# Kernel optimization log

Hardware: AMD Instinct MI355X
Metric: run time of the kernel (lower is better)

## Reference

```python
import jax, jax.numpy as jnp
import numpy as np
import math

B, T, C = 2, 2048, 1024
H = 16
HD = C // H  # 64
LAMBDA_INIT = 0.7 - 0.6 * math.exp(-0.3 * (2 - 1))
EPS = 1e-5


def setup_inputs() -> dict:
    key = jax.random.key(0)
    ks = jax.random.split(key, 12)
    s = 1.0 / math.sqrt(C)
    return {
        'x':   jax.random.normal(ks[0], (B, T, C), jnp.float32),
        'Wq1': jax.random.normal(ks[1], (C, C), jnp.float32) * s,
        'Wq2': jax.random.normal(ks[2], (C, C), jnp.float32) * s,
        'Wk1': jax.random.normal(ks[3], (C, C), jnp.float32) * s,
        'Wk2': jax.random.normal(ks[4], (C, C), jnp.float32) * s,
        'Wv':  jax.random.normal(ks[5], (2 * C, C), jnp.float32) * s,
        'Wc':  jax.random.normal(ks[6], (C, 2 * C), jnp.float32) * (1.0 / math.sqrt(2 * C)),
        'lq1': jax.random.normal(ks[7], (H, HD), jnp.float32) * 0.1,
        'lk1': jax.random.normal(ks[8], (H, HD), jnp.float32) * 0.1,
        'lq2': jax.random.normal(ks[9], (H, HD), jnp.float32) * 0.1,
        'lk2': jax.random.normal(ks[10], (H, HD), jnp.float32) * 0.1,
    }


def _heads(x, W, d):
    # x:[B,T,C] @ W.T:[C,out] -> [B,H,T,d]
    b, t, _ = x.shape
    return jnp.einsum('btc,dc->btd', x, W).reshape(b, t, H, d).transpose(0, 2, 1, 3)


def reference(x, Wq1, Wq2, Wk1, Wk2, Wv, Wc, lq1, lk1, lq2, lk2):
    b, t, c = x.shape
    q1 = _heads(x, Wq1, HD)
    q2 = _heads(x, Wq2, HD)
    k1 = _heads(x, Wk1, HD)
    k2 = _heads(x, Wk2, HD)
    v = _heads(x, Wv, 2 * HD)  # [B,H,T,2hd]
    scale = 1.0 / math.sqrt(HD)
    causal = jnp.tril(jnp.ones((t, t), bool))  # [T,T]
    neg = jnp.float32(-jnp.inf)
    att1 = jnp.einsum('bhqd,bhkd->bhqk', q1, k1) * scale
    att2 = jnp.einsum('bhqd,bhkd->bhqk', q2, k2) * scale
    att1 = jax.nn.softmax(jnp.where(causal, att1, neg), axis=-1)
    att2 = jax.nn.softmax(jnp.where(causal, att2, neg), axis=-1)
    lam1 = jnp.exp(jnp.sum(lq1 * lk1, -1))  # [H]
    lam2 = jnp.exp(jnp.sum(lq2 * lk2, -1))
    lam_full = (lam1 - lam2 + LAMBDA_INIT)[None, :, None, None]
    att = att1 - lam_full * att2
    y = jnp.einsum('bhqk,bhkd->bhqd', att, v)  # [B,H,T,2hd]
    # sub-layernorm over last dim, no affine
    mu = jnp.mean(y, -1, keepdims=True)
    var = jnp.mean(jnp.square(y - mu), -1, keepdims=True)
    y = (y - mu) * jax.lax.rsqrt(var + EPS)
    y = y * (1.0 - LAMBDA_INIT)
    y = y.transpose(0, 2, 1, 3).reshape(b, t, 2 * c)
    return jnp.einsum('btd,cd->btc', y, Wc)
```

## Files before the change

kernel.cpp:

```cpp
#include <hip/hip_runtime.h>
#include <stdint.h>

typedef unsigned short u16;
typedef unsigned int   u32;
typedef short  short8  __attribute__((ext_vector_type(8)));
typedef float  f32x4   __attribute__((ext_vector_type(4)));
typedef u16    u16x4   __attribute__((ext_vector_type(4)));
typedef u32    u32x4   __attribute__((ext_vector_type(4)));

#define LAMBDA_INIT   0.25550906759096927f
#define ONE_MINUS_LI  0.7444909324090307f
#define QSCALE        0.18033688011112043f

__device__ __forceinline__ u16 f2bf(float f) {
  union { float f; u32 u; } v; v.f = f;
  u32 r = v.u + 0x7fffu + ((v.u >> 16) & 1u);
  return (u16)(r >> 16);
}

__device__ __forceinline__ u32 packtr(float a, float b) {
  return (__builtin_bit_cast(u32, a) >> 16) | (__builtin_bit_cast(u32, b) & 0xffff0000u);
}

__device__ __forceinline__ float expv(float x) {
  float r; asm("v_exp_f32 %0, %1" : "=v"(r) : "v"(x)); return r;
}

__device__ __forceinline__ void gload16(const void* g, void* l) {
  __builtin_amdgcn_global_load_lds(
      (const __attribute__((address_space(1))) void*)g,
      (__attribute__((address_space(3))) void*)l, 16, 0, 0);
}

__global__ __launch_bounds__(256) void k_cvt(const float* __restrict__ s,
                                             u16* __restrict__ d, int n) {
  int i = (blockIdx.x * 256 + threadIdx.x) * 4;
  if (i >= n) return;
  float4 v = *(const float4*)(s + i);
  u16x4 o = { f2bf(v.x), f2bf(v.y), f2bf(v.z), f2bf(v.w) };
  *(u16x4*)(d + i) = o;
}

__global__ __launch_bounds__(256) void k_cvt4(
    const float* __restrict__ s0, const float* __restrict__ s1,
    const float* __restrict__ s2, const float* __restrict__ s3,
    u16* __restrict__ d) {
  const float* s = (blockIdx.y == 0) ? s0 : (blockIdx.y == 1) ? s1
                 : (blockIdx.y == 2) ? s2 : s3;
  int i = (blockIdx.x * 256 + threadIdx.x) * 4;
  float4 v = *(const float4*)(s + i);
  u16x4 o = { f2bf(v.x), f2bf(v.y), f2bf(v.z), f2bf(v.w) };
  *(u16x4*)(d + blockIdx.y * 1048576 + i) = o;
}

__device__ __forceinline__ void gemm_tile_128(
    const u16* __restrict__ A, const u16* __restrict__ Bm, int K,
    int m0, int n0, char* smem, f32x4 acc[4][4]) {
  const int tid = threadIdx.x;
  const int l = tid & 63, w = tid >> 6, g = l >> 4, q = l & 15;
  const int wm = w >> 1, wn = w & 1;
  char* As = smem;
  char* Bs = smem + 16384;
#pragma unroll
  for (int mi = 0; mi < 4; mi++)
#pragma unroll
    for (int ni = 0; ni < 4; ni++) acc[mi][ni] = (f32x4){0.f, 0.f, 0.f, 0.f};

  const int nkt = K >> 6;
  for (int kt = 0; kt < nkt; ++kt) {
    __syncthreads();
#pragma unroll
    for (int i = 0; i < 4; i++) {
      int cc = i * 256 + tid;
      int row = cc >> 3, off = cc & 7;
      int sw = (off * 16) ^ ((row & 7) << 4);
      gload16((const char*)A + ((size_t)(m0 + row) * K + kt * 64) * 2 + sw, As + cc * 16);
      gload16((const char*)Bm + ((size_t)(n0 + row) * K + kt * 64) * 2 + sw, Bs + cc * 16);
    }
    __syncthreads();
#pragma unroll
    for (int ks = 0; ks < 2; ++ks) {
      short8 af[4], bf[4];
#pragma unroll
      for (int mi = 0; mi < 4; mi++) {
        int row = wm * 64 + mi * 16 + q;
        af[mi] = *(const short8*)(As + ((row * 128 + ks * 64 + g * 16) ^ ((row & 7) << 4)));
      }
#pragma unroll
      for (int ni = 0; ni < 4; ni++) {
        int row = wn * 64 + ni * 16 + q;
        bf[ni] = *(const short8*)(Bs + ((row * 128 + ks * 64 + g * 16) ^ ((row & 7) << 4)));
      }
#pragma unroll
      for (int mi = 0; mi < 4; mi++)
#pragma unroll
        for (int ni = 0; ni < 4; ni++)
          acc[mi][ni] = __builtin_amdgcn_mfma_f32_16x16x32_bf16(af[mi], bf[ni], acc[mi][ni], 0, 0, 0);
    }
  }
}

__global__ __launch_bounds__(256) void k_gemm_qkv(
    const u16* __restrict__ xb, const u16* __restrict__ wall,
    u16* __restrict__ q1, u16* __restrict__ q2,
    u16* __restrict__ k1, u16* __restrict__ k2,
    u16* __restrict__ vt) {
  __shared__ __align__(16) char smem[32768];
  f32x4 acc[4][4];
  const int n0 = blockIdx.x * 128, m0 = blockIdx.y * 128;
  gemm_tile_128(xb, wall, 1024, m0, n0, smem, acc);

  const int l = threadIdx.x & 63, w = threadIdx.x >> 6, g = l >> 4, q = l & 15;
  const int wm = w >> 1, wn = w & 1;
  const int seg = n0 >> 10;
  const float sc = (seg < 2) ? QSCALE : 1.0f;
  u16* qk = (seg == 0) ? q1 : (seg == 1) ? q2 : (seg == 2) ? k1 : k2;
#pragma unroll
  for (int mi = 0; mi < 4; mi++)
#pragma unroll
    for (int ni = 0; ni < 4; ni++) {
      int row0 = m0 + wm * 64 + mi * 16 + 4 * g;
      int col = n0 + wn * 64 + ni * 16 + q;
      int bb = row0 >> 11;
      if (seg < 4) {
        int h = (col >> 6) & 15, hd = col & 63;
#pragma unroll
        for (int r = 0; r < 4; r++) {
          int t = (row0 + r) & 2047;
          qk[(((size_t)bb * 16 + h) * 2048 + t) * 64 + hd] = f2bf(acc[mi][ni][r] * sc);
        }
      } else {
        int nv = col - 4096, hh = nv >> 7, d = nv & 127;
        int t = row0 & 2047;
        u16x4 pv;
#pragma unroll
        for (int r = 0; r < 4; r++) pv[r] = f2bf(acc[mi][ni][r]);
        size_t addr = (size_t)(bb * 16 + hh) * 262144 + (size_t)(t >> 6) * 8192
                    + (size_t)(((((t >> 5) & 1) * 8 + (d >> 4)) * 512)
                               + ((t >> 3) & 3) * 128 + (d & 15) * 8 + (t & 7));
        *(u16x4*)(vt + addr) = pv;
      }
    }
}

__global__ __launch_bounds__(256) void k_attn(
    const u16* __restrict__ q1p, const u16* __restrict__ q2p,
    const u16* __restrict__ k1p, const u16* __restrict__ k2p,
    const u16* __restrict__ vfp,
    const float* __restrict__ lq1, const float* __restrict__ lk1,
    const float* __restrict__ lq2, const float* __restrict__ lk2,
    u16* __restrict__ ybp) {
  __shared__ __align__(16) char smem[65536];
  const int bh = blockIdx.y, b = bh >> 4, h = bh & 15;
  const int tid = threadIdx.x, w = tid >> 6, l = tid & 63, g = l >> 4, q = l & 15;
  const int xA = blockIdx.x;
  const int nA = xA + 1;

  float a1 = lq1[h * 64 + l] * lk1[h * 64 + l];
  float a2 = lq2[h * 64 + l] * lk2[h * 64 + l];
#pragma unroll
  for (int off = 32; off; off >>= 1) {
    a1 += __shfl_xor(a1, off);
    a2 += __shfl_xor(a2, off);
  }
  const float lam = expf(a1) - expf(a2) + LAMBDA_INIT;

  short8 qf[2][2];
  f32x4 o[2][8];
  float lsum[2];
  int qrow = 0;

  auto init_tile = [&](int q0) {
    qrow = q0 + w * 16 + q;
    size_t qoff = ((size_t)bh * 2048 + qrow) * 64;
#pragma unroll
    for (int ks = 0; ks < 2; ++ks) {
      qf[0][ks] = *(const short8*)(q1p + qoff + ks * 32 + g * 8);
      qf[1][ks] = *(const short8*)(q2p + qoff + ks * 32 + g * 8);
    }
#pragma unroll
    for (int s = 0; s < 2; s++) {
      lsum[s] = 0.f;
#pragma unroll
      for (int mt = 0; mt < 8; mt++) o[s][mt] = (f32x4){0.f, 0.f, 0.f, 0.f};
    }
  };

  auto stage_kv = [&](char* sb, int kv0) {
#pragma unroll
    for (int i = 0; i < 2; i++) {
      int cc = i * 256 + tid, kv = cc >> 3, off = cc & 7;
      int sw = (off * 16) ^ ((kv & 7) << 4);
      size_t rb = ((size_t)bh * 2048 + kv0 + kv) * 128;
      gload16((const char*)k1p + rb + sw, sb + cc * 16);
      gload16((const char*)k2p + rb + sw, sb + 8192 + cc * 16);
    }
    const char* vsrc = (const char*)vfp + (size_t)bh * 524288 + (size_t)(kv0 >> 6) * 16384;
#pragma unroll
    for (int i = 0; i < 4; i++) {
      int cc = i * 256 + tid;
      gload16(vsrc + cc * 16, sb + 16384 + cc * 16);
    }
  };

  auto epilogue = [&]() {
    float l0 = lsum[0]; l0 += __shfl_xor(l0, 16); l0 += __shfl_xor(l0, 32);
    float l1 = lsum[1]; l1 += __shfl_xor(l1, 16); l1 += __shfl_xor(l1, 32);
    const float inv0 = 1.f / l0, inv1 = 1.f / l1;
    float sum = 0.f, ssq = 0.f;
#pragma unroll
    for (int mt = 0; mt < 8; ++mt)
#pragma unroll
      for (int r = 0; r < 4; r++) {
        float y = o[0][mt][r] * inv0 - lam * (o[1][mt][r] * inv1);
        o[0][mt][r] = y;
        sum += y;
        ssq += y * y;
      }
    sum += __shfl_xor(sum, 16); sum += __shfl_xor(sum, 32);
    ssq += __shfl_xor(ssq, 16); ssq += __shfl_xor(ssq, 32);
    const float mean = sum * (1.f / 128.f);
    const float var = ssq * (1.f / 128.f) - mean * mean;
    const float rstd = rsqrtf(var + 1e-5f) * ONE_MINUS_LI;
    u16* dst = ybp + ((size_t)(b * 2048 + qrow)) * 2048 + h * 128;
#pragma unroll
    for (int mt = 0; mt < 8; ++mt) {
      u16x4 pv;
#pragma unroll
      for (int r = 0; r < 4; r++) pv[r] = f2bf((o[0][mt][r] - mean) * rstd);
      *(u16x4*)(dst + mt * 16 + 4 * g) = pv;
    }
  };

  init_tile(xA * 64);
  stage_kv(smem, 0);

  for (int i = 0; i < 33; ++i) {
    char* sb = smem + (i & 1) * 32768;
    asm volatile("s_waitcnt vmcnt(0)" ::: "memory");
    __builtin_amdgcn_s_barrier();
    if (i + 1 < 33) {
      int kvn = (i + 1 < nA) ? (i + 1) * 64 : (i + 1 - nA) * 64;
      stage_kv(smem + ((i + 1) & 1) * 32768, kvn);
    }

    const int kv0 = (i < nA) ? i * 64 : (i - nA) * 64;
    const bool diag = (i == nA - 1) || (i == 32);

#pragma unroll
    for (int kk = 0; kk < 2; ++kk) {
      u32 pk[2][4];
#pragma unroll
      for (int s = 0; s < 2; ++s) {
        const char* Ks = sb + s * 8192;
        f32x4 s0 = {0.f, 0.f, 0.f, 0.f}, s1 = {0.f, 0.f, 0.f, 0.f};
#pragma unroll
        for (int ks = 0; ks < 2; ++ks) {
          short8 af0 = *(const short8*)(Ks + (((kk * 32 + q) * 128 + ks * 64 + g * 16) ^ ((q & 7) << 4)));
          short8 af1 = *(const short8*)(Ks + (((kk * 32 + 16 + q) * 128 + ks * 64 + g * 16) ^ ((q & 7) << 4)));
          s0 = __builtin_amdgcn_mfma_f32_16x16x32_bf16(af0, qf[s][ks], s0, 0, 0, 0);
          s1 = __builtin_amdgcn_mfma_f32_16x16x32_bf16(af1, qf[s][ks], s1, 0, 0, 0);
        }
        const int kb0 = kv0 + kk * 32 + 4 * g, kb1 = kb0 + 16;
        if (diag) {
#pragma unroll
          for (int r = 0; r < 4; r++) {
            s0[r] = (kb0 + r > qrow) ? -1e30f : s0[r];
            s1[r] = (kb1 + r > qrow) ? -1e30f : s1[r];
          }
        }
        float p0[4], p1[4], rs = 0.f;
#pragma unroll
        for (int r = 0; r < 4; r++) {
          p0[r] = expv(s0[r]);
          p1[r] = expv(s1[r]);
          rs += p0[r] + p1[r];
        }
        lsum[s] += rs;

        u32 pk0[2] = { packtr(p0[0], p0[1]), packtr(p0[2], p0[3]) };
        u32 pk1[2] = { packtr(p1[0], p1[1]), packtr(p1[2], p1[3]) };
        int srcA = q + (g & 1) * 32;
        int srcB = srcA + 16;
        u32 xa0 = (u32)__shfl((int)pk0[0], srcA), xa1 = (u32)__shfl((int)pk0[1], srcA);
        u32 xa2 = (u32)__shfl((int)pk0[0], srcB), xa3 = (u32)__shfl((int)pk0[1], srcB);
        u32 xb0 = (u32)__shfl((int)pk1[0], srcA), xb1 = (u32)__shfl((int)pk1[1], srcA);
        u32 xb2 = (u32)__shfl((int)pk1[0], srcB), xb3 = (u32)__shfl((int)pk1[1], srcB);
        bool lo = (g < 2);
        pk[s][0] = lo ? xa0 : xb0;
        pk[s][1] = lo ? xa1 : xb1;
        pk[s][2] = lo ? xa2 : xb2;
        pk[s][3] = lo ? xa3 : xb3;
      }
      u32x4 t0 = {pk[0][0], pk[0][1], pk[0][2], pk[0][3]};
      u32x4 t1 = {pk[1][0], pk[1][1], pk[1][2], pk[1][3]};
      short8 pf0 = __builtin_bit_cast(short8, t0);
      short8 pf1 = __builtin_bit_cast(short8, t1);
      const char* Vb = sb + 16384 + kk * 8192 + l * 16;
#pragma unroll
      for (int mt = 0; mt < 8; ++mt) {
        short8 vf = *(const short8*)(Vb + mt * 1024);
        o[0][mt] = __builtin_amdgcn_mfma_f32_16x16x32_bf16(vf, pf0, o[0][mt], 0, 0, 0);
        o[1][mt] = __builtin_amdgcn_mfma_f32_16x16x32_bf16(vf, pf1, o[1][mt], 0, 0, 0);
      }
    }

    if (i == nA - 1) {
      epilogue();
      init_tile((31 - xA) * 64);
    }
  }
  epilogue();
}

__global__ __launch_bounds__(256) void k_gemm_out(
    const u16* __restrict__ yb, const u16* __restrict__ wcb,
    float* __restrict__ out) {
  __shared__ __align__(16) char smem[32768];
  f32x4 acc[4][4];
  const int n0 = blockIdx.x * 128, m0 = blockIdx.y * 128;
  gemm_tile_128(yb, wcb, 2048, m0, n0, smem, acc);
  const int l = threadIdx.x & 63, w = threadIdx.x >> 6, g = l >> 4, q = l & 15;
  const int wm = w >> 1, wn = w & 1;
#pragma unroll
  for (int mi = 0; mi < 4; mi++)
#pragma unroll
    for (int ni = 0; ni < 4; ni++)
#pragma unroll
      for (int r = 0; r < 4; r++) {
        int row = m0 + wm * 64 + mi * 16 + 4 * g + r;
        int col = n0 + wn * 64 + ni * 16 + q;
        out[(size_t)row * 1024 + col] = acc[mi][ni][r];
      }
}

extern "C" void kernel_launch(void* const* d_in, const int* in_sizes, int n_in,
                              void* d_out, int out_size, void* d_ws, size_t ws_size,
                              hipStream_t stream) {
  const float* x   = (const float*)d_in[0];
  const float* Wq1 = (const float*)d_in[1];
  const float* Wq2 = (const float*)d_in[2];
  const float* Wk1 = (const float*)d_in[3];
  const float* Wk2 = (const float*)d_in[4];
  const float* Wv  = (const float*)d_in[5];
  const float* Wc  = (const float*)d_in[6];
  const float* lq1 = (const float*)d_in[7];
  const float* lk1 = (const float*)d_in[8];
  const float* lq2 = (const float*)d_in[9];
  const float* lk2 = (const float*)d_in[10];

  char* ws = (char*)d_ws;
  u16* xb   = (u16*)(ws);
  u16* wall = (u16*)(ws + 8388608);
  u16* wcb  = (u16*)(ws + 20971520);
  u16* q1   = (u16*)(ws + 25165824);
  u16* q2   = (u16*)(ws + 33554432);
  u16* k1   = (u16*)(ws + 41943040);
  u16* k2   = (u16*)(ws + 50331648);
  u16* vt   = (u16*)(ws + 58720256);
  u16* yb   = (u16*)(ws + 75497472);

  k_cvt<<<4096, 256, 0, stream>>>(x, xb, 4194304);
  k_cvt4<<<dim3(1024, 4), 256, 0, stream>>>(Wq1, Wq2, Wk1, Wk2, wall);
  k_cvt<<<2048, 256, 0, stream>>>(Wv,  wall + 4194304,  2097152);
  k_cvt<<<2048, 256, 0, stream>>>(Wc,  wcb, 2097152);

  k_gemm_qkv<<<dim3(48, 32), 256, 0, stream>>>(xb, wall, q1, q2, k1, k2, vt);
  k_attn<<<dim3(16, 32), 256, 0, stream>>>(q1, q2, k1, k2, vt,
                                           lq1, lk1, lq2, lk2, yb);
  k_gemm_out<<<dim3(8, 32), 256, 0, stream>>>(yb, wcb, (float*)d_out);
}
```

Before: 225.0 us.

## Use 512-thread attention blocks over 128-row query tiles, heavy tiles first

Before, each 256-thread block handled a pair of 64-row query tiles (x and 31-x) to balance causal work. Now each block has 8 waves covering one 128-row query tile. Tiles are scheduled in reverse order so the longest causal tiles start first, and each K/V chunk staged in shared memory is shared by twice as many query rows. Waves whose rows lie entirely before a chunk skip its compute but still join the barriers. Per-block work is now unbalanced, and the launch bounds of 512 threads with 4 blocks per CU limit registers.

Measured after the change: 473.7 us. 111% more time.

```diff
diff --git a/kernel.cpp b/kernel.cpp
--- a/kernel.cpp
+++ b/kernel.cpp
@@ -143,7 +143,7 @@
     }
 }
 
-__global__ __launch_bounds__(256) void k_attn(
+__global__ __launch_bounds__(512, 4) void k_attn(
     const u16* __restrict__ q1p, const u16* __restrict__ q2p,
     const u16* __restrict__ k1p, const u16* __restrict__ k2p,
     const u16* __restrict__ vfp,
@@ -153,8 +153,11 @@
   __shared__ __align__(16) char smem[65536];
   const int bh = blockIdx.y, b = bh >> 4, h = bh & 15;
   const int tid = threadIdx.x, w = tid >> 6, l = tid & 63, g = l >> 4, q = l & 15;
-  const int xA = blockIdx.x;
-  const int nA = xA + 1;
+  const int tile = 15 - blockIdx.x;
+  const int base = tile * 128;
+  const int nchunk = 2 * tile + 2;
+  const int qrow = base + w * 16 + q;
+  const int wqmin = base + w * 16;
 
   float a1 = lq1[h * 64 + l] * lk1[h * 64 + l];
   float a2 = lq2[h * 64 + l] * lk2[h * 64 + l];
@@ -166,86 +169,43 @@
   const float lam = expf(a1) - expf(a2) + LAMBDA_INIT;
 
   short8 qf[2][2];
-  f32x4 o[2][8];
-  float lsum[2];
-  int qrow = 0;
-
-  auto init_tile = [&](int q0) {
-    qrow = q0 + w * 16 + q;
+  {
     size_t qoff = ((size_t)bh * 2048 + qrow) * 64;
 #pragma unroll
     for (int ks = 0; ks < 2; ++ks) {
       qf[0][ks] = *(const short8*)(q1p + qoff + ks * 32 + g * 8);
       qf[1][ks] = *(const short8*)(q2p + qoff + ks * 32 + g * 8);
     }
-#pragma unroll
-    for (int s = 0; s < 2; s++) {
-      lsum[s] = 0.f;
-#pragma unroll
-      for (int mt = 0; mt < 8; mt++) o[s][mt] = (f32x4){0.f, 0.f, 0.f, 0.f};
-    }
+  }
+  f32x4 o[2][8];
+  float lsum[2] = {0.f, 0.f};
+#pragma unroll
+  for (int s = 0; s < 2; s++)
+#pragma unroll
+    for (int mt = 0; mt < 8; mt++) o[s][mt] = (f32x4){0.f, 0.f, 0.f, 0.f};
+
+  auto stage_kv = [&](char* sb, int kv0) {
+    int kv = tid >> 3, off = tid & 7;
+    int sw = (off * 16) ^ ((kv & 7) << 4);
+    size_t rb = ((size_t)bh * 2048 + kv0 + kv) * 128;
+    gload16((const char*)k1p + rb + sw, sb + tid * 16);
+    gload16((const char*)k2p + rb + sw, sb + 8192 + tid * 16);
+    const char* vsrc = (const char*)vfp + (size_t)bh * 524288 + (size_t)(kv0 >> 6) * 16384;
+    gload16(vsrc + tid * 16, sb + 16384 + tid * 16);
+    gload16(vsrc + 8192 + tid * 16, sb + 24576 + tid * 16);
   };
 
-  auto stage_kv = [&](char* sb, int kv0) {
-#pragma unroll
-    for (int i = 0; i < 2; i++) {
-      int cc = i * 256 + tid, kv = cc >> 3, off = cc & 7;
-      int sw = (off * 16) ^ ((kv & 7) << 4);
-      size_t rb = ((size_t)bh * 2048 + kv0 + kv) * 128;
-      gload16((const char*)k1p + rb + sw, sb + cc * 16);
-      gload16((const char*)k2p + rb + sw, sb + 8192 + cc * 16);
-    }
-    const char* vsrc = (const char*)vfp + (size_t)bh * 524288 + (size_t)(kv0 >> 6) * 16384;
-#pragma unroll
-    for (int i = 0; i < 4; i++) {
-      int cc = i * 256 + tid;
-      gload16(vsrc + cc * 16, sb + 16384 + cc * 16);
-    }
-  };
-
-  auto epilogue = [&]() {
-    float l0 = lsum[0]; l0 += __shfl_xor(l0, 16); l0 += __shfl_xor(l0, 32);
-    float l1 = lsum[1]; l1 += __shfl_xor(l1, 16); l1 += __shfl_xor(l1, 32);
-    const float inv0 = 1.f / l0, inv1 = 1.f / l1;
-    float sum = 0.f, ssq = 0.f;
-#pragma unroll
-    for (int mt = 0; mt < 8; ++mt)
-#pragma unroll
-      for (int r = 0; r < 4; r++) {
-        float y = o[0][mt][r] * inv0 - lam * (o[1][mt][r] * inv1);
-        o[0][mt][r] = y;
-        sum += y;
-        ssq += y * y;
-      }
-    sum += __shfl_xor(sum, 16); sum += __shfl_xor(sum, 32);
-    ssq += __shfl_xor(ssq, 16); ssq += __shfl_xor(ssq, 32);
-    const float mean = sum * (1.f / 128.f);
-    const float var = ssq * (1.f / 128.f) - mean * mean;
-    const float rstd = rsqrtf(var + 1e-5f) * ONE_MINUS_LI;
-    u16* dst = ybp + ((size_t)(b * 2048 + qrow)) * 2048 + h * 128;
-#pragma unroll
-    for (int mt = 0; mt < 8; ++mt) {
-      u16x4 pv;
-#pragma unroll
-      for (int r = 0; r < 4; r++) pv[r] = f2bf((o[0][mt][r] - mean) * rstd);
-      *(u16x4*)(dst + mt * 16 + 4 * g) = pv;
-    }
-  };
-
-  init_tile(xA * 64);
   stage_kv(smem, 0);
 
-  for (int i = 0; i < 33; ++i) {
-    char* sb = smem + (i & 1) * 32768;
+  for (int c = 0; c < nchunk; ++c) {
+    char* sb = smem + (c & 1) * 32768;
     asm volatile("s_waitcnt vmcnt(0)" ::: "memory");
     __builtin_amdgcn_s_barrier();
-    if (i + 1 < 33) {
-      int kvn = (i + 1 < nA) ? (i + 1) * 64 : (i + 1 - nA) * 64;
-      stage_kv(smem + ((i + 1) & 1) * 32768, kvn);
-    }
-
-    const int kv0 = (i < nA) ? i * 64 : (i - nA) * 64;
-    const bool diag = (i == nA - 1) || (i == 32);
+    if (c + 1 < nchunk) stage_kv(smem + ((c + 1) & 1) * 32768, (c + 1) * 64);
+
+    const int kv0 = c * 64;
+    if (kv0 > wqmin + 15) continue;
+    const bool diag = (kv0 + 63 > wqmin);
 
 #pragma unroll
     for (int kk = 0; kk < 2; ++kk) {
@@ -304,13 +264,34 @@
         o[1][mt] = __builtin_amdgcn_mfma_f32_16x16x32_bf16(vf, pf1, o[1][mt], 0, 0, 0);
       }
     }
-
-    if (i == nA - 1) {
-      epilogue();
-      init_tile((31 - xA) * 64);
-    }
-  }
-  epilogue();
+  }
+
+  float l0 = lsum[0]; l0 += __shfl_xor(l0, 16); l0 += __shfl_xor(l0, 32);
+  float l1 = lsum[1]; l1 += __shfl_xor(l1, 16); l1 += __shfl_xor(l1, 32);
+  const float inv0 = 1.f / l0, inv1 = 1.f / l1;
+  float sum = 0.f, ssq = 0.f;
+#pragma unroll
+  for (int mt = 0; mt < 8; ++mt)
+#pragma unroll
+    for (int r = 0; r < 4; r++) {
+      float y = o[0][mt][r] * inv0 - lam * (o[1][mt][r] * inv1);
+      o[0][mt][r] = y;
+      sum += y;
+      ssq += y * y;
+    }
+  sum += __shfl_xor(sum, 16); sum += __shfl_xor(sum, 32);
+  ssq += __shfl_xor(ssq, 16); ssq += __shfl_xor(ssq, 32);
+  const float mean = sum * (1.f / 128.f);
+  const float var = ssq * (1.f / 128.f) - mean * mean;
+  const float rstd = rsqrtf(var + 1e-5f) * ONE_MINUS_LI;
+  u16* dst = ybp + ((size_t)(b * 2048 + qrow)) * 2048 + h * 128;
+#pragma unroll
+  for (int mt = 0; mt < 8; ++mt) {
+    u16x4 pv;
+#pragma unroll
+    for (int r = 0; r < 4; r++) pv[r] = f2bf((o[0][mt][r] - mean) * rstd);
+    *(u16x4*)(dst + mt * 16 + 4 * g) = pv;
+  }
 }
 
 __global__ __launch_bounds__(256) void k_gemm_out(
@@ -366,7 +347,7 @@
   k_cvt<<<2048, 256, 0, stream>>>(Wc,  wcb, 2097152);
 
   k_gemm_qkv<<<dim3(48, 32), 256, 0, stream>>>(xb, wall, q1, q2, k1, k2, vt);
-  k_attn<<<dim3(16, 32), 256, 0, stream>>>(q1, q2, k1, k2, vt,
+  k_attn<<<dim3(16, 32), 512, 0, stream>>>(q1, q2, k1, k2, vt,
                                            lq1, lk1, lq2, lk2, yb);
   k_gemm_out<<<dim3(8, 32), 256, 0, stream>>>(yb, wcb, (float*)d_out);
 }
```

## Merge conversion kernels into one launch and use 512-thread output GEMM

Applied to the files above, without the earlier changes.

The four fp32-to-bf16 conversion launches become a single 12-segment kernel, which cuts launch overhead and lets all conversions run in one wave. The output projection GEMM now uses 512 threads (8 waves) per 128x128 tile, so each wave computes a 32x64 sub-tile and holds half the accumulators. The intent is more waves per CU and better latency hiding for a grid of only 256 blocks. In exchange, each wave reuses its LDS fragments less and per-block barrier cost rises.

Result: faster. 213.0 us (-5.3%).

```diff
diff --git a/kernel.cpp b/kernel.cpp
--- a/kernel.cpp
+++ b/kernel.cpp
@@ -32,25 +32,26 @@
       (__attribute__((address_space(3))) void*)l, 16, 0, 0);
 }
 
-__global__ __launch_bounds__(256) void k_cvt(const float* __restrict__ s,
-                                             u16* __restrict__ d, int n) {
+__global__ __launch_bounds__(256) void k_cvt12(
+    const float* __restrict__ x,  const float* __restrict__ wq1,
+    const float* __restrict__ wq2, const float* __restrict__ wk1,
+    const float* __restrict__ wk2, const float* __restrict__ wv,
+    const float* __restrict__ wc,
+    u16* __restrict__ xb, u16* __restrict__ wall, u16* __restrict__ wcb) {
+  const int seg = blockIdx.y;
+  const float* s;
+  u16* d;
+  if (seg < 4)       { s = x + (size_t)seg * 1048576;        d = xb + (size_t)seg * 1048576; }
+  else if (seg == 4) { s = wq1;                              d = wall; }
+  else if (seg == 5) { s = wq2;                              d = wall + 1048576; }
+  else if (seg == 6) { s = wk1;                              d = wall + 2097152; }
+  else if (seg == 7) { s = wk2;                              d = wall + 3145728; }
+  else if (seg < 10) { s = wv + (size_t)(seg - 8) * 1048576; d = wall + 4194304 + (size_t)(seg - 8) * 1048576; }
+  else               { s = wc + (size_t)(seg - 10) * 1048576; d = wcb + (size_t)(seg - 10) * 1048576; }
   int i = (blockIdx.x * 256 + threadIdx.x) * 4;
-  if (i >= n) return;
   float4 v = *(const float4*)(s + i);
   u16x4 o = { f2bf(v.x), f2bf(v.y), f2bf(v.z), f2bf(v.w) };
   *(u16x4*)(d + i) = o;
-}
-
-__global__ __launch_bounds__(256) void k_cvt4(
-    const float* __restrict__ s0, const float* __restrict__ s1,
-    const float* __restrict__ s2, const float* __restrict__ s3,
-    u16* __restrict__ d) {
-  const float* s = (blockIdx.y == 0) ? s0 : (blockIdx.y == 1) ? s1
-                 : (blockIdx.y == 2) ? s2 : s3;
-  int i = (blockIdx.x * 256 + threadIdx.x) * 4;
-  float4 v = *(const float4*)(s + i);
-  u16x4 o = { f2bf(v.x), f2bf(v.y), f2bf(v.z), f2bf(v.w) };
-  *(u16x4*)(d + blockIdx.y * 1048576 + i) = o;
 }
 
 __device__ __forceinline__ void gemm_tile_128(
@@ -313,22 +314,60 @@
   epilogue();
 }
 
-__global__ __launch_bounds__(256) void k_gemm_out(
+__global__ __launch_bounds__(512) void k_gemm_out(
     const u16* __restrict__ yb, const u16* __restrict__ wcb,
     float* __restrict__ out) {
   __shared__ __align__(16) char smem[32768];
-  f32x4 acc[4][4];
+  const int tid = threadIdx.x;
+  const int l = tid & 63, w = tid >> 6, g = l >> 4, q = l & 15;
+  const int wm = w >> 1, wn = w & 1;
   const int n0 = blockIdx.x * 128, m0 = blockIdx.y * 128;
-  gemm_tile_128(yb, wcb, 2048, m0, n0, smem, acc);
-  const int l = threadIdx.x & 63, w = threadIdx.x >> 6, g = l >> 4, q = l & 15;
-  const int wm = w >> 1, wn = w & 1;
-#pragma unroll
-  for (int mi = 0; mi < 4; mi++)
+  char* As = smem;
+  char* Bs = smem + 16384;
+  f32x4 acc[2][4];
+#pragma unroll
+  for (int mi = 0; mi < 2; mi++)
+#pragma unroll
+    for (int ni = 0; ni < 4; ni++) acc[mi][ni] = (f32x4){0.f, 0.f, 0.f, 0.f};
+
+  for (int kt = 0; kt < 32; ++kt) {
+    __syncthreads();
+#pragma unroll
+    for (int i = 0; i < 2; i++) {
+      int cc = i * 512 + tid;
+      int row = cc >> 3, off = cc & 7;
+      int sw = (off * 16) ^ ((row & 7) << 4);
+      gload16((const char*)yb + ((size_t)(m0 + row) * 2048 + kt * 64) * 2 + sw, As + cc * 16);
+      gload16((const char*)wcb + ((size_t)(n0 + row) * 2048 + kt * 64) * 2 + sw, Bs + cc * 16);
+    }
+    __syncthreads();
+#pragma unroll
+    for (int ks = 0; ks < 2; ++ks) {
+      short8 af[2], bf[4];
+#pragma unroll
+      for (int mi = 0; mi < 2; mi++) {
+        int row = wm * 32 + mi * 16 + q;
+        af[mi] = *(const short8*)(As + ((row * 128 + ks * 64 + g * 16) ^ ((row & 7) << 4)));
+      }
+#pragma unroll
+      for (int ni = 0; ni < 4; ni++) {
+        int row = wn * 64 + ni * 16 + q;
+        bf[ni] = *(const short8*)(Bs + ((row * 128 + ks * 64 + g * 16) ^ ((row & 7) << 4)));
+      }
+#pragma unroll
+      for (int mi = 0; mi < 2; mi++)
+#pragma unroll
+        for (int ni = 0; ni < 4; ni++)
+          acc[mi][ni] = __builtin_amdgcn_mfma_f32_16x16x32_bf16(af[mi], bf[ni], acc[mi][ni], 0, 0, 0);
+    }
+  }
+#pragma unroll
+  for (int mi = 0; mi < 2; mi++)
 #pragma unroll
     for (int ni = 0; ni < 4; ni++)
 #pragma unroll
       for (int r = 0; r < 4; r++) {
-        int row = m0 + wm * 64 + mi * 16 + 4 * g + r;
+        int row = m0 + wm * 32 + mi * 16 + 4 * g + r;
         int col = n0 + wn * 64 + ni * 16 + q;
         out[(size_t)row * 1024 + col] = acc[mi][ni][r];
       }
@@ -360,13 +399,10 @@
   u16* vt   = (u16*)(ws + 58720256);
   u16* yb   = (u16*)(ws + 75497472);
 
-  k_cvt<<<4096, 256, 0, stream>>>(x, xb, 4194304);
-  k_cvt4<<<dim3(1024, 4), 256, 0, stream>>>(Wq1, Wq2, Wk1, Wk2, wall);
-  k_cvt<<<2048, 256, 0, stream>>>(Wv,  wall + 4194304,  2097152);
-  k_cvt<<<2048, 256, 0, stream>>>(Wc,  wcb, 2097152);
-
+  k_cvt12<<<dim3(1024, 12), 256, 0, stream>>>(x, Wq1, Wq2, Wk1, Wk2, Wv, Wc,
+                                              xb, wall, wcb);
   k_gemm_qkv<<<dim3(48, 32), 256, 0, stream>>>(xb, wall, q1, q2, k1, k2, vt);
   k_attn<<<dim3(16, 32), 256, 0, stream>>>(q1, q2, k1, k2, vt,
                                            lq1, lk1, lq2, lk2, yb);
-  k_gemm_out<<<dim3(8, 32), 256, 0, stream>>>(yb, wcb, (float*)d_out);
-}
+  k_gemm_out<<<dim3(8, 32), 512, 0, stream>>>(yb, wcb, (float*)d_out);
+}
```
